# Performance work log

Hardware: AMD Instinct MI355X
Metric: run time of the kernel (lower is better)

## Reference

```python
import jax, jax.numpy as jnp
import numpy as np

N = 10000   # num nodes (== num_features, source uses identity features)
H = 4       # attention heads
F = 128     # out_features per head (concat=False -> mean over heads)
E = 320000  # directed edges
SLOPE = 0.2 # PyG GATConv default negative_slope


def setup_inputs() -> dict:
    key = jax.random.key(0)
    ks = jax.random.split(key, 20)
    inp = {}
    inp['x'] = jax.random.normal(ks[0], (N, N), jnp.float32)
    inp['edge_index'] = jax.random.randint(ks[1], (2, E), 0, N, dtype=jnp.int64)
    dims = [N, F, F, F]
    k = 2
    for i, din in enumerate(dims):
        inp[f'W{i}'] = jax.random.normal(ks[k], (din, H * F), jnp.float32) / np.sqrt(din).astype(np.float32); k += 1
        inp[f'as{i}'] = jax.random.normal(ks[k], (H, F), jnp.float32) / np.sqrt(F).astype(np.float32); k += 1
        inp[f'ad{i}'] = jax.random.normal(ks[k], (H, F), jnp.float32) / np.sqrt(F).astype(np.float32); k += 1
        inp[f'b{i}'] = jnp.zeros((F,), jnp.float32)
    return inp


def _gat_layer(x, src, dst, W, a_src, a_dst, b):
    # x: [N, Din]; W: [Din, H*F]; a_src/a_dst: [H, F]; b: [F]
    h = (x @ W).reshape(-1, H, F)                      # [N, H, F]
    al_s = jnp.sum(h * a_src, axis=-1)                 # [N, H]
    al_d = jnp.sum(h * a_dst, axis=-1)                 # [N, H]
    e = jax.nn.leaky_relu(al_s[src] + al_d[dst], SLOPE)  # [E', H]
    # segment softmax over edges grouped by target node
    m = jax.ops.segment_max(e, dst, num_segments=N)    # [N, H]
    ex = jnp.exp(e - m[dst])
    s = jax.ops.segment_sum(ex, dst, num_segments=N)   # [N, H]
    alpha = ex / s[dst]                                 # [E', H]
    msg = h[src] * alpha[:, :, None]                    # [E', H, F]
    out = jax.ops.segment_sum(msg, dst, num_segments=N) # [N, H, F]
    return out.mean(axis=1) + b                         # concat=False: head mean + bias


def reference(x, edge_index, W0, W1, W2, W3, as0, as1, as2, as3,
              ad0, ad1, ad2, ad3, b0, b1, b2, b3):
    # add self-loops once (PyG GATConv add_self_loops=True, same each layer)
    loop = jnp.arange(N, dtype=edge_index.dtype)
    src = jnp.concatenate([edge_index[0], loop])
    dst = jnp.concatenate([edge_index[1], loop])

    h = jax.nn.relu(_gat_layer(x, src, dst, W0, as0, ad0, b0))
    h = jax.nn.relu(_gat_layer(h, src, dst, W1, as1, ad1, b1))
    h = jax.nn.relu(_gat_layer(h, src, dst, W2, as2, ad2, b2))
    z = jnp.tanh(_gat_layer(h, src, dst, W3, as3, ad3, b3))   # encode
    adj_recon = jax.nn.sigmoid(z @ z.T)                       # decode, [N, N]
    return adj_recon, z
```

## Files before the change

### kernel.cpp

```cpp
#include <hip/hip_runtime.h>

#define N_ 10000
#define H_ 4
#define F_ 128
#define HF_ 512
#define E_ 320000
#define EN_ 330000

typedef unsigned short u16;
typedef __attribute__((ext_vector_type(8))) short bf16x8;
typedef __attribute__((ext_vector_type(4))) float f32x4;

__device__ __forceinline__ u16 f2b1(float f) {
  return (u16)((__float_as_uint(f) + 0x8000u) >> 16);
}
__device__ __forceinline__ unsigned int f2b2(float a, float b) {
  unsigned int ua = __float_as_uint(a) + 0x8000u;
  unsigned int ub = __float_as_uint(b) + 0x8000u;
  return (ua >> 16) | (ub & 0xffff0000u);
}
__device__ __forceinline__ float b2f(u16 u) {
  return __uint_as_float(((unsigned int)u) << 16);
}
__device__ __forceinline__ void async_cp16(const void* g, void* l) {
  __builtin_amdgcn_global_load_lds((__attribute__((address_space(1))) void*)g,
                                   (__attribute__((address_space(3))) void*)l,
                                   16, 0, 0);
}

__global__ void transpose_f2b(const float* __restrict__ in, u16* __restrict__ out,
                              int R, int C) {
  __shared__ float t[32][33];
  int bx = blockIdx.x * 32, by = blockIdx.y * 32;
  int tx = threadIdx.x, ty = threadIdx.y;
#pragma unroll
  for (int i = 0; i < 32; i += 8) {
    int r = by + ty + i, c = bx + tx;
    if (r < R && c < C) t[ty + i][tx] = in[(size_t)r * C + c];
  }
  __syncthreads();
#pragma unroll
  for (int i = 0; i < 32; i += 8) {
    int c = bx + ty + i, r = by + tx;
    if (r < R && c < C) out[(size_t)c * R + r] = f2b1(t[tx][ty + i]);
  }
}

__global__ void zero_k(int* __restrict__ p, int n) {
  int t = blockIdx.x * blockDim.x + threadIdx.x;
  if (t < n) p[t] = 0;
}
__global__ void hist_k(const int* __restrict__ ei, int* __restrict__ cnt) {
  int t = blockIdx.x * blockDim.x + threadIdx.x;
  if (t >= EN_) return;
  int d = (t < E_) ? ei[E_ + t] : (t - E_);
  atomicAdd(&cnt[d], 1);
}
__global__ void scan_k(const int* __restrict__ cnt, int* __restrict__ rp) {
  __shared__ int l[1024];
  const int CH = 10;
  int t = threadIdx.x;
  int base = t * CH;
  int loc[CH];
  int s = 0;
#pragma unroll
  for (int i = 0; i < CH; ++i) {
    int idx = base + i;
    int c = (idx < N_) ? cnt[idx] : 0;
    loc[i] = s; s += c;
  }
  l[t] = s;
  __syncthreads();
  for (int off = 1; off < 1024; off <<= 1) {
    int v = (t >= off) ? l[t - off] : 0;
    __syncthreads();
    l[t] += v;
    __syncthreads();
  }
  int cb = (t == 0) ? 0 : l[t - 1];
#pragma unroll
  for (int i = 0; i < CH; ++i) {
    int idx = base + i;
    if (idx < N_) rp[idx] = cb + loc[i];
  }
  if (t == 1023) rp[N_] = l[1023];
}
__global__ void fill_k(const int* __restrict__ ei, const int* __restrict__ rp,
                       int* __restrict__ fl, int* __restrict__ csrc) {
  int t = blockIdx.x * blockDim.x + threadIdx.x;
  if (t >= EN_) return;
  int s, d;
  if (t < E_) { s = ei[t]; d = ei[E_ + t]; } else { s = d = t - E_; }
  int pos = rp[d] + atomicAdd(&fl[d], 1);
  csrc[pos] = s;
}

#define MFMA_STEP()                                                           \
  {                                                                           \
    bf16x8 af[4], bv[4];                                                      \
    _Pragma("unroll") for (int i = 0; i < 4; ++i)                             \
        af[i] = *(const bf16x8*)&As[(wm + i * 16 + l16) * 32 + quad * 8];     \
    _Pragma("unroll") for (int j = 0; j < 4; ++j)                             \
        bv[j] = *(const bf16x8*)&Bs[(wn + j * 16 + l16) * 32 + quad * 8];     \
    _Pragma("unroll") for (int i = 0; i < 4; ++i)                             \
        _Pragma("unroll") for (int j = 0; j < 4; ++j)                         \
            acc[i][j] = __builtin_amdgcn_mfma_f32_16x16x32_bf16(              \
                af[i], bv[j], acc[i][j], 0, 0, 0);                            \
  }

template <int ASRC, int MODE, int SPLIT>
__global__ __launch_bounds__(256) void gemm_k(const void* __restrict__ Av,
                                              const u16* __restrict__ Bt,
                                              float* __restrict__ C,
                                              int M, int Nc, int K) {
  __shared__ u16 As[128 * 32];
  __shared__ u16 Bs[128 * 32];
  const int tid = threadIdx.x;
  const int lane = tid & 63, wave = tid >> 6;
  const int wm = (wave >> 1) * 64, wn = (wave & 1) * 64;
  const int l16 = lane & 15, quad = lane >> 4;
  const int mBase = blockIdx.y * 128, nBase = blockIdx.x * 128;
  const int r0 = tid >> 2, kk = (tid & 3) * 8;

  int k0 = 0, k1 = K;
  if (SPLIT) {
    int Kper = ((K + (int)gridDim.z - 1) / (int)gridDim.z + 31) & ~31;
    k0 = blockIdx.z * Kper;
    k1 = min(K, k0 + Kper);
    if (k0 > k1) k0 = k1;
  }
  const int len = k1 - k0;

  const u16* Ab = (const u16*)Av;
  const float* Af = (const float*)Av;

  size_t ar0 = (size_t)min(mBase + r0, M - 1);
  size_t ar1 = (size_t)min(mBase + r0 + 64, M - 1);
  size_t br0 = (size_t)min(nBase + r0, Nc - 1);
  size_t br1 = (size_t)min(nBase + r0 + 64, Nc - 1);
  const u16* pb0 = Bt + br0 * (size_t)K + k0 + kk;
  const u16* pb1 = Bt + br1 * (size_t)K + k0 + kk;
  const u16* pa0 = Ab + ar0 * (size_t)K + k0 + kk;
  const u16* pa1 = Ab + ar1 * (size_t)K + k0 + kk;
  const float* pf0 = Af + ar0 * (size_t)K + k0 + kk;
  const float* pf1 = Af + ar1 * (size_t)K + k0 + kk;
  u16* lA0 = As + wave * 512;
  u16* lA1 = As + 2048 + wave * 512;
  u16* lB0 = Bs + wave * 512;
  u16* lB1 = Bs + 2048 + wave * 512;

  f32x4 acc[4][4];
  f32x4 zr = {0.f, 0.f, 0.f, 0.f};
#pragma unroll
  for (int i = 0; i < 4; ++i)
#pragma unroll
    for (int j = 0; j < 4; ++j) acc[i][j] = zr;

  const int Lmain = len & ~31;
  for (int kb = 0; kb < Lmain; kb += 32) {
    async_cp16(pb0 + kb, lB0);
    async_cp16(pb1 + kb, lB1);
    if (ASRC == 0) {
      async_cp16(pa0 + kb, lA0);
      async_cp16(pa1 + kb, lA1);
    } else {
      float4 x0 = *(const float4*)(pf0 + kb);
      float4 x1 = *(const float4*)(pf0 + kb + 4);
      float4 x2 = *(const float4*)(pf1 + kb);
      float4 x3 = *(const float4*)(pf1 + kb + 4);
      uint4 u0 = make_uint4(f2b2(x0.x, x0.y), f2b2(x0.z, x0.w),
                            f2b2(x1.x, x1.y), f2b2(x1.z, x1.w));
      uint4 u1 = make_uint4(f2b2(x2.x, x2.y), f2b2(x2.z, x2.w),
                            f2b2(x3.x, x3.y), f2b2(x3.z, x3.w));
      *(uint4*)&As[r0 * 32 + kk] = u0;
      *(uint4*)&As[(r0 + 64) * 32 + kk] = u1;
    }
    __syncthreads();
    MFMA_STEP();
    __syncthreads();
  }
  if (len & 31) {
#pragma unroll
    for (int c = 0; c < 2; ++c) {
      size_t gr = c ? ar1 : ar0;
      size_t gb = c ? br1 : br0;
      int lrow = r0 + c * 64;
#pragma unroll
      for (int j = 0; j < 8; ++j) {
        int k = k0 + Lmain + kk + j;
        u16 av = 0, bvv = 0;
        if (k < k1) {
          av = (ASRC == 1) ? f2b1(Af[gr * (size_t)K + k]) : Ab[gr * (size_t)K + k];
          bvv = Bt[gb * (size_t)K + k];
        }
        As[lrow * 32 + kk + j] = av;
        Bs[lrow * 32 + kk + j] = bvv;
      }
    }
    __syncthreads();
    MFMA_STEP();
  }

  float* Cw = SPLIT ? (C + (size_t)blockIdx.z * (size_t)M * (size_t)Nc) : C;
#pragma unroll
  for (int i = 0; i < 4; ++i)
#pragma unroll
    for (int j = 0; j < 4; ++j)
#pragma unroll
      for (int r = 0; r < 4; ++r) {
        int row = mBase + wm + i * 16 + quad * 4 + r;
        int col = nBase + wn + j * 16 + l16;
        if (row < M && col < Nc) {
          float v = acc[i][j][r];
          if (!SPLIT && MODE == 1) v = 1.f / (1.f + __expf(-v));
          Cw[(size_t)row * Nc + col] = v;
        }
      }
}

__global__ __launch_bounds__(256) void reduce_k(const float* __restrict__ part,
                                                float* __restrict__ out,
                                                int nq, int S) {
  int t = blockIdx.x * blockDim.x + threadIdx.x;
  if (t >= nq) return;
  size_t stride = (size_t)nq * 4;
  float4 s = ((const float4*)part)[t];
#pragma unroll 1
  for (int z = 1; z < S; ++z) {
    float4 v = *(const float4*)(part + (size_t)z * stride + (size_t)t * 4);
    s.x += v.x; s.y += v.y; s.z += v.z; s.w += v.w;
  }
  ((float4*)out)[t] = s;
}

__global__ __launch_bounds__(256) void prep_k(const float* __restrict__ h,
                                              const float* __restrict__ asv,
                                              const float* __restrict__ adv,
                                              u16* __restrict__ h2,
                                              float* __restrict__ als,
                                              float* __restrict__ ald) {
  int wave = threadIdx.x >> 6, lane = threadIdx.x & 63;
  int node = blockIdx.x * 4 + wave;
  if (node >= N_) return;
  const float* hp = h + (size_t)node * HF_;
  float4 v0 = ((const float4*)hp)[lane * 2];
  float4 v1 = ((const float4*)hp)[lane * 2 + 1];
  float vv[8] = {v0.x, v0.y, v0.z, v0.w, v1.x, v1.y, v1.z, v1.w};
  uint4 pk = make_uint4(f2b2(vv[0], vv[1]), f2b2(vv[2], vv[3]),
                        f2b2(vv[4], vv[5]), f2b2(vv[6], vv[7]));
  *(uint4*)&h2[(size_t)node * HF_ + lane * 8] = pk;
  float4 a0 = ((const float4*)(asv + lane * 8))[0];
  float4 a1 = ((const float4*)(asv + lane * 8))[1];
  float4 d0 = ((const float4*)(adv + lane * 8))[0];
  float4 d1 = ((const float4*)(adv + lane * 8))[1];
  float aa[8] = {a0.x, a0.y, a0.z, a0.w, a1.x, a1.y, a1.z, a1.w};
  float dd[8] = {d0.x, d0.y, d0.z, d0.w, d1.x, d1.y, d1.z, d1.w};
  float ss = 0.f, sd = 0.f;
#pragma unroll
  for (int j = 0; j < 8; ++j) {
    ss += vv[j] * aa[j];
    sd += vv[j] * dd[j];
  }
#pragma unroll
  for (int m = 1; m <= 8; m <<= 1) {
    ss += __shfl_xor(ss, m, 64);
    sd += __shfl_xor(sd, m, 64);
  }
  if ((lane & 15) == 0) {
    int hh = lane >> 4;
    als[node * 4 + hh] = ss;
    ald[node * 4 + hh] = sd;
  }
}

__global__ __launch_bounds__(256) void agg_k(const u16* __restrict__ h2,
                                             const float* __restrict__ als,
                                             const float* __restrict__ ald,
                                             const int* __restrict__ rp,
                                             const int* __restrict__ csrc,
                                             const float* __restrict__ bias,
                                             u16* __restrict__ xout,
                                             float* __restrict__ z32, int act) {
  __shared__ float red[1024];
  __shared__ float sh[512];
  int n = blockIdx.x, t = threadIdx.x;
  int start = rp[n], end = rp[n + 1];
  int hh = t >> 6;
  float4 ad4 = *(const float4*)&ald[n * 4];
  float adh[4] = {ad4.x, ad4.y, ad4.z, ad4.w};
  float lm[4] = {-1e30f, -1e30f, -1e30f, -1e30f};
  for (int j = start + t; j < end; j += 256) {
    int s = csrc[j];
    float4 a4 = *(const float4*)&als[s * 4];
    float e0 = a4.x + adh[0]; e0 = e0 > 0.f ? e0 : 0.2f * e0;
    float e1 = a4.y + adh[1]; e1 = e1 > 0.f ? e1 : 0.2f * e1;
    float e2 = a4.z + adh[2]; e2 = e2 > 0.f ? e2 : 0.2f * e2;
    float e3 = a4.w + adh[3]; e3 = e3 > 0.f ? e3 : 0.2f * e3;
    lm[0] = fmaxf(lm[0], e0); lm[1] = fmaxf(lm[1], e1);
    lm[2] = fmaxf(lm[2], e2); lm[3] = fmaxf(lm[3], e3);
  }
#pragma unroll
  for (int h = 0; h < 4; ++h) red[t * 4 + h] = lm[h];
  __syncthreads();
  for (int off = 128; off >= 1; off >>= 1) {
    if (t < off) {
#pragma unroll
      for (int h = 0; h < 4; ++h)
        red[t * 4 + h] = fmaxf(red[t * 4 + h], red[(t + off) * 4 + h]);
    }
    __syncthreads();
  }
  float mh = red[hh];
  float adhh = adh[hh];
  float acc0 = 0.f, acc1 = 0.f, ssum = 0.f;
  for (int j = start; j < end; ++j) {
    int s = csrc[j];
    float e = als[s * 4 + hh] + adhh;
    e = e > 0.f ? e : 0.2f * e;
    float w = __expf(e - mh);
    ssum += w;
    unsigned int p = *(const unsigned int*)&h2[(size_t)s * HF_ + 2 * t];
    acc0 += w * b2f((u16)(p & 0xffffu));
    acc1 += w * b2f((u16)(p >> 16));
  }
  float inv = 1.f / ssum;
  sh[2 * t] = acc0 * inv;
  sh[2 * t + 1] = acc1 * inv;
  __syncthreads();
  if (t < 64) {
    int f0 = 2 * t, f1 = 2 * t + 1;
    float w0 = 0.25f * (sh[f0] + sh[128 + f0] + sh[256 + f0] + sh[384 + f0]) + bias[f0];
    float w1 = 0.25f * (sh[f1] + sh[128 + f1] + sh[256 + f1] + sh[384 + f1]) + bias[f1];
    if (act) { w0 = tanhf(w0); w1 = tanhf(w1); }
    else     { w0 = fmaxf(w0, 0.f); w1 = fmaxf(w1, 0.f); }
    if (z32) {
      z32[(size_t)n * F_ + f0] = w0;
      z32[(size_t)n * F_ + f1] = w1;
    }
    *(unsigned int*)&xout[(size_t)n * F_ + f0] = f2b2(w0, w1);
  }
}

extern "C" void kernel_launch(void* const* d_in, const int* in_sizes, int n_in,
                              void* d_out, int out_size, void* d_ws, size_t ws_size,
                              hipStream_t stream) {
  const float* x = (const float*)d_in[0];
  const int* ei = (const int*)d_in[1];
  const float* W[4]; const float* asv[4]; const float* adv[4]; const float* bv[4];
  for (int i = 0; i < 4; ++i) {
    W[i]   = (const float*)d_in[2 + i * 4];
    asv[i] = (const float*)d_in[3 + i * 4];
    adv[i] = (const float*)d_in[4 + i * 4];
    bv[i]  = (const float*)d_in[5 + i * 4];
  }
  float* out_adj = (float*)d_out;
  float* out_z = out_adj + (size_t)N_ * N_;

  char* w = (char*)d_ws;
  size_t o = 0;
  auto carve = [&](size_t bytes) {
    char* p = w + o;
    o += (bytes + 255) & ~(size_t)255;
    return p;
  };
  float* hbuf = (float*)carve((size_t)N_ * HF_ * 4);
  u16* h2   = (u16*)carve((size_t)N_ * HF_ * 2);
  u16* wt0  = (u16*)carve((size_t)HF_ * N_ * 2);
  u16* wt1  = (u16*)carve((size_t)HF_ * F_ * 2);
  u16* wt2  = (u16*)carve((size_t)HF_ * F_ * 2);
  u16* wt3  = (u16*)carve((size_t)HF_ * F_ * 2);
  float* als = (float*)carve((size_t)N_ * 4 * 4);
  float* ald = (float*)carve((size_t)N_ * 4 * 4);
  u16* bufA = (u16*)carve((size_t)N_ * F_ * 2);
  u16* bufB = (u16*)carve((size_t)N_ * F_ * 2);
  u16* zb   = (u16*)carve((size_t)N_ * F_ * 2);
  int* cnt = (int*)carve((size_t)2 * N_ * 4);
  int* fl = cnt + N_;
  int* rowptr = (int*)carve((size_t)(N_ + 1) * 4);
  int* csrc = (int*)carve((size_t)EN_ * 4);

  const int SPLITK = 8;
  float* part = out_adj;

  dim3 tb(32, 8);
  transpose_f2b<<<dim3(16, 313), tb, 0, stream>>>(W[0], wt0, N_, HF_);
  transpose_f2b<<<dim3(16, 4), tb, 0, stream>>>(W[1], wt1, F_, HF_);
  transpose_f2b<<<dim3(16, 4), tb, 0, stream>>>(W[2], wt2, F_, HF_);
  transpose_f2b<<<dim3(16, 4), tb, 0, stream>>>(W[3], wt3, F_, HF_);

  zero_k<<<(2 * N_ + 255) / 256, 256, 0, stream>>>(cnt, 2 * N_);
  hist_k<<<(EN_ + 255) / 256, 256, 0, stream>>>(ei, cnt);
  scan_k<<<1, 1024, 0, stream>>>(cnt, rowptr);
  fill_k<<<(EN_ + 255) / 256, 256, 0, stream>>>(ei, rowptr, fl, csrc);

  const u16* wt[4] = {wt0, wt1, wt2, wt3};
  const u16* xin[4] = {nullptr, bufA, bufB, bufA};
  u16* xout[4] = {bufA, bufB, bufA, zb};

  for (int l = 0; l < 4; ++l) {
    if (l == 0) {
      gemm_k<1, 0, 1><<<dim3(4, 79, SPLITK), 256, 0, stream>>>(x, wt0, part,
                                                               N_, HF_, N_);
      int nq = N_ * HF_ / 4;
      reduce_k<<<(nq + 255) / 256, 256, 0, stream>>>(part, hbuf, nq, SPLITK);
    } else {
      gemm_k<0, 0, 0><<<dim3(4, 79), 256, 0, stream>>>(xin[l], wt[l], hbuf,
                                                       N_, HF_, F_);
    }
    prep_k<<<N_ / 4, 256, 0, stream>>>(hbuf, asv[l], adv[l], h2, als, ald);
    agg_k<<<N_, 256, 0, stream>>>(h2, als, ald, rowptr, csrc, bv[l], xout[l],
                                  (l == 3) ? out_z : nullptr, (l == 3) ? 1 : 0);
  }

  gemm_k<0, 1, 0><<<dim3(79, 79), 256, 0, stream>>>(zb, zb, out_adj, N_, N_, F_);
}
```

Before: 1.421 ms.

## Pre-convert input to bf16 and fuse split-K reduction into prep kernel

Adds a standalone kernel that converts the large fp32 input matrix to bf16 once, so the first-layer GEMM loads A tiles with async global-to-LDS copies instead of converting fp32 inline per tile. The split-K partial sums are now reduced inside the prep kernel, which removes the separate reduce kernel and its extra full-size write and read. Scratch buffers are placed in the output adjacency buffer, which the final GEMM overwrites. The cost is an extra full pass over the input for conversion.

```diff
diff --git a/kernel.cpp b/kernel.cpp
--- a/kernel.cpp
+++ b/kernel.cpp
@@ -26,6 +26,19 @@
   __builtin_amdgcn_global_load_lds((__attribute__((address_space(1))) void*)g,
                                    (__attribute__((address_space(3))) void*)l,
                                    16, 0, 0);
+}
+
+__global__ __launch_bounds__(256) void convert_k(const float* __restrict__ in,
+                                                 u16* __restrict__ out, long nq) {
+  long t = (long)blockIdx.x * blockDim.x + threadIdx.x;
+  long stride = (long)gridDim.x * blockDim.x;
+  for (long i = t; i < nq; i += stride) {
+    float4 a = ((const float4*)in)[i * 2];
+    float4 b = ((const float4*)in)[i * 2 + 1];
+    uint4 p = make_uint4(f2b2(a.x, a.y), f2b2(a.z, a.w),
+                         f2b2(b.x, b.y), f2b2(b.z, b.w));
+    ((uint4*)out)[i] = p;
+  }
 }
 
 __global__ void transpose_f2b(const float* __restrict__ in, u16* __restrict__ out,
@@ -108,8 +121,8 @@
                 af[i], bv[j], acc[i][j], 0, 0, 0);                            \
   }
 
-template <int ASRC, int MODE, int SPLIT>
-__global__ __launch_bounds__(256) void gemm_k(const void* __restrict__ Av,
+template <int MODE, int SPLIT>
+__global__ __launch_bounds__(256) void gemm_k(const u16* __restrict__ Ab,
                                               const u16* __restrict__ Bt,
                                               float* __restrict__ C,
                                               int M, int Nc, int K) {
@@ -131,9 +144,6 @@
   }
   const int len = k1 - k0;
 
-  const u16* Ab = (const u16*)Av;
-  const float* Af = (const float*)Av;
-
   size_t ar0 = (size_t)min(mBase + r0, M - 1);
   size_t ar1 = (size_t)min(mBase + r0 + 64, M - 1);
   size_t br0 = (size_t)min(nBase + r0, Nc - 1);
@@ -142,8 +152,6 @@
   const u16* pb1 = Bt + br1 * (size_t)K + k0 + kk;
   const u16* pa0 = Ab + ar0 * (size_t)K + k0 + kk;
   const u16* pa1 = Ab + ar1 * (size_t)K + k0 + kk;
-  const float* pf0 = Af + ar0 * (size_t)K + k0 + kk;
-  const float* pf1 = Af + ar1 * (size_t)K + k0 + kk;
   u16* lA0 = As + wave * 512;
   u16* lA1 = As + 2048 + wave * 512;
   u16* lB0 = Bs + wave * 512;
@@ -160,21 +168,8 @@
   for (int kb = 0; kb < Lmain; kb += 32) {
     async_cp16(pb0 + kb, lB0);
     async_cp16(pb1 + kb, lB1);
-    if (ASRC == 0) {
-      async_cp16(pa0 + kb, lA0);
-      async_cp16(pa1 + kb, lA1);
-    } else {
-      float4 x0 = *(const float4*)(pf0 + kb);
-      float4 x1 = *(const float4*)(pf0 + kb + 4);
-      float4 x2 = *(const float4*)(pf1 + kb);
-      float4 x3 = *(const float4*)(pf1 + kb + 4);
-      uint4 u0 = make_uint4(f2b2(x0.x, x0.y), f2b2(x0.z, x0.w),
-                            f2b2(x1.x, x1.y), f2b2(x1.z, x1.w));
-      uint4 u1 = make_uint4(f2b2(x2.x, x2.y), f2b2(x2.z, x2.w),
-                            f2b2(x3.x, x3.y), f2b2(x3.z, x3.w));
-      *(uint4*)&As[r0 * 32 + kk] = u0;
-      *(uint4*)&As[(r0 + 64) * 32 + kk] = u1;
-    }
+    async_cp16(pa0 + kb, lA0);
+    async_cp16(pa1 + kb, lA1);
     __syncthreads();
     MFMA_STEP();
     __syncthreads();
@@ -190,7 +185,7 @@
         int k = k0 + Lmain + kk + j;
         u16 av = 0, bvv = 0;
         if (k < k1) {
-          av = (ASRC == 1) ? f2b1(Af[gr * (size_t)K + k]) : Ab[gr * (size_t)K + k];
+          av = Ab[gr * (size_t)K + k];
           bvv = Bt[gb * (size_t)K + k];
         }
         As[lrow * 32 + kk + j] = av;
@@ -218,33 +213,27 @@
       }
 }
 
-__global__ __launch_bounds__(256) void reduce_k(const float* __restrict__ part,
-                                                float* __restrict__ out,
-                                                int nq, int S) {
-  int t = blockIdx.x * blockDim.x + threadIdx.x;
-  if (t >= nq) return;
-  size_t stride = (size_t)nq * 4;
-  float4 s = ((const float4*)part)[t];
-#pragma unroll 1
-  for (int z = 1; z < S; ++z) {
-    float4 v = *(const float4*)(part + (size_t)z * stride + (size_t)t * 4);
-    s.x += v.x; s.y += v.y; s.z += v.z; s.w += v.w;
-  }
-  ((float4*)out)[t] = s;
-}
-
 __global__ __launch_bounds__(256) void prep_k(const float* __restrict__ h,
                                               const float* __restrict__ asv,
                                               const float* __restrict__ adv,
                                               u16* __restrict__ h2,
                                               float* __restrict__ als,
-                                              float* __restrict__ ald) {
+                                              float* __restrict__ ald,
+                                              int S, size_t zstride) {
   int wave = threadIdx.x >> 6, lane = threadIdx.x & 63;
   int node = blockIdx.x * 4 + wave;
   if (node >= N_) return;
   const float* hp = h + (size_t)node * HF_;
   float4 v0 = ((const float4*)hp)[lane * 2];
   float4 v1 = ((const float4*)hp)[lane * 2 + 1];
+#pragma unroll 1
+  for (int z = 1; z < S; ++z) {
+    const float* pp = hp + (size_t)z * zstride;
+    float4 w0 = ((const float4*)pp)[lane * 2];
+    float4 w1 = ((const float4*)pp)[lane * 2 + 1];
+    v0.x += w0.x; v0.y += w0.y; v0.z += w0.z; v0.w += w0.w;
+    v1.x += w1.x; v1.y += w1.y; v1.z += w1.z; v1.w += w1.w;
+  }
   float vv[8] = {v0.x, v0.y, v0.z, v0.w, v1.x, v1.y, v1.z, v1.w};
   uint4 pk = make_uint4(f2b2(vv[0], vv[1]), f2b2(vv[2], vv[3]),
                         f2b2(vv[4], vv[5]), f2b2(vv[6], vv[7]));
@@ -380,7 +369,8 @@
   int* csrc = (int*)carve((size_t)EN_ * 4);
 
   const int SPLITK = 8;
-  float* part = out_adj;
+  u16* xb = (u16*)out_adj;
+  float* part = out_adj + (size_t)N_ * N_ / 2;
 
   dim3 tb(32, 8);
   transpose_f2b<<<dim3(16, 313), tb, 0, stream>>>(W[0], wt0, N_, HF_);
@@ -388,6 +378,8 @@
   transpose_f2b<<<dim3(16, 4), tb, 0, stream>>>(W[2], wt2, F_, HF_);
   transpose_f2b<<<dim3(16, 4), tb, 0, stream>>>(W[3], wt3, F_, HF_);
 
+  convert_k<<<2048, 256, 0, stream>>>(x, xb, (long)N_ * N_ / 8);
+
   zero_k<<<(2 * N_ + 255) / 256, 256, 0, stream>>>(cnt, 2 * N_);
   hist_k<<<(EN_ + 255) / 256, 256, 0, stream>>>(ei, cnt);
   scan_k<<<1, 1024, 0, stream>>>(cnt, rowptr);
@@ -399,18 +391,19 @@
 
   for (int l = 0; l < 4; ++l) {
     if (l == 0) {
-      gemm_k<1, 0, 1><<<dim3(4, 79, SPLITK), 256, 0, stream>>>(x, wt0, part,
-                                                               N_, HF_, N_);
-      int nq = N_ * HF_ / 4;
-      reduce_k<<<(nq + 255) / 256, 256, 0, stream>>>(part, hbuf, nq, SPLITK);
+      gemm_k<0, 1><<<dim3(4, 79, SPLITK), 256, 0, stream>>>(xb, wt0, part,
+                                                            N_, HF_, N_);
+      prep_k<<<N_ / 4, 256, 0, stream>>>(part, asv[0], adv[0], h2, als, ald,
+                                         SPLITK, (size_t)N_ * HF_);
     } else {
-      gemm_k<0, 0, 0><<<dim3(4, 79), 256, 0, stream>>>(xin[l], wt[l], hbuf,
-                                                       N_, HF_, F_);
+      gemm_k<0, 0><<<dim3(4, 79), 256, 0, stream>>>(xin[l], wt[l], hbuf,
+                                                    N_, HF_, F_);
+      prep_k<<<N_ / 4, 256, 0, stream>>>(hbuf, asv[l], adv[l], h2, als, ald,
+                                         1, 0);
     }
-    prep_k<<<N_ / 4, 256, 0, stream>>>(hbuf, asv[l], adv[l], h2, als, ald);
     agg_k<<<N_, 256, 0, stream>>>(h2, als, ald, rowptr, csrc, bv[l], xout[l],
                                   (l == 3) ? out_z : nullptr, (l == 3) ? 1 : 0);
   }
 
-  gemm_k<0, 1, 0><<<dim3(79, 79), 256, 0, stream>>>(zb, zb, out_adj, N_, N_, F_);
-}
+  gemm_k<1, 0><<<dim3(79, 79), 256, 0, stream>>>(zb, zb, out_adj, N_, N_, F_);
+}
```

New measurement: 1.508 ms. 1.06x slower.

## Double-buffer GEMM shared tiles and fold split-K reduction into prep kernel

Applied to the files above, without the earlier changes.

The GEMM kernel now uses two shared-memory tile buffers, so the next K-tile is loaded (async copies, or fp32 loads converted to bf16 after the MFMAs) while the current tile is computed. This leaves one barrier per iteration instead of two. The separate split-K reduce kernel is removed: prep_k sums the partial slices directly, saving a full write and reread of the N×512 fp32 intermediate and one launch. Shared memory per block doubles, which may lower occupancy.

```diff
diff --git a/kernel.cpp b/kernel.cpp
--- a/kernel.cpp
+++ b/kernel.cpp
@@ -95,13 +95,13 @@
   csrc[pos] = s;
 }
 
-#define MFMA_STEP()                                                           \
+#define MFMA_TILE(ASP, BSP)                                                   \
   {                                                                           \
     bf16x8 af[4], bv[4];                                                      \
     _Pragma("unroll") for (int i = 0; i < 4; ++i)                             \
-        af[i] = *(const bf16x8*)&As[(wm + i * 16 + l16) * 32 + quad * 8];     \
+        af[i] = *(const bf16x8*)&(ASP)[(wm + i * 16 + l16) * 32 + quad * 8];  \
     _Pragma("unroll") for (int j = 0; j < 4; ++j)                             \
-        bv[j] = *(const bf16x8*)&Bs[(wn + j * 16 + l16) * 32 + quad * 8];     \
+        bv[j] = *(const bf16x8*)&(BSP)[(wn + j * 16 + l16) * 32 + quad * 8];  \
     _Pragma("unroll") for (int i = 0; i < 4; ++i)                             \
         _Pragma("unroll") for (int j = 0; j < 4; ++j)                         \
             acc[i][j] = __builtin_amdgcn_mfma_f32_16x16x32_bf16(              \
@@ -113,8 +113,8 @@
                                               const u16* __restrict__ Bt,
                                               float* __restrict__ C,
                                               int M, int Nc, int K) {
-  __shared__ u16 As[128 * 32];
-  __shared__ u16 Bs[128 * 32];
+  __shared__ u16 As[2][128 * 32];
+  __shared__ u16 Bs[2][128 * 32];
   const int tid = threadIdx.x;
   const int lane = tid & 63, wave = tid >> 6;
   const int wm = (wave >> 1) * 64, wn = (wave & 1) * 64;
@@ -144,10 +144,8 @@
   const u16* pa1 = Ab + ar1 * (size_t)K + k0 + kk;
   const float* pf0 = Af + ar0 * (size_t)K + k0 + kk;
   const float* pf1 = Af + ar1 * (size_t)K + k0 + kk;
-  u16* lA0 = As + wave * 512;
-  u16* lA1 = As + 2048 + wave * 512;
-  u16* lB0 = Bs + wave * 512;
-  u16* lB1 = Bs + 2048 + wave * 512;
+  const int lofsA = wave * 512;
+  const int lofsA2 = 2048 + wave * 512;
 
   f32x4 acc[4][4];
   f32x4 zr = {0.f, 0.f, 0.f, 0.f};
@@ -157,28 +155,59 @@
     for (int j = 0; j < 4; ++j) acc[i][j] = zr;
 
   const int Lmain = len & ~31;
-  for (int kb = 0; kb < Lmain; kb += 32) {
-    async_cp16(pb0 + kb, lB0);
-    async_cp16(pb1 + kb, lB1);
+  const int nt = Lmain >> 5;
+
+  if (nt > 0) {
+    async_cp16(pb0, Bs[0] + lofsA);
+    async_cp16(pb1, Bs[0] + lofsA2);
     if (ASRC == 0) {
-      async_cp16(pa0 + kb, lA0);
-      async_cp16(pa1 + kb, lA1);
+      async_cp16(pa0, As[0] + lofsA);
+      async_cp16(pa1, As[0] + lofsA2);
     } else {
-      float4 x0 = *(const float4*)(pf0 + kb);
-      float4 x1 = *(const float4*)(pf0 + kb + 4);
-      float4 x2 = *(const float4*)(pf1 + kb);
-      float4 x3 = *(const float4*)(pf1 + kb + 4);
-      uint4 u0 = make_uint4(f2b2(x0.x, x0.y), f2b2(x0.z, x0.w),
-                            f2b2(x1.x, x1.y), f2b2(x1.z, x1.w));
-      uint4 u1 = make_uint4(f2b2(x2.x, x2.y), f2b2(x2.z, x2.w),
-                            f2b2(x3.x, x3.y), f2b2(x3.z, x3.w));
-      *(uint4*)&As[r0 * 32 + kk] = u0;
-      *(uint4*)&As[(r0 + 64) * 32 + kk] = u1;
-    }
-    __syncthreads();
-    MFMA_STEP();
-    __syncthreads();
-  }
+      float4 x0 = *(const float4*)(pf0);
+      float4 x1 = *(const float4*)(pf0 + 4);
+      float4 x2 = *(const float4*)(pf1);
+      float4 x3 = *(const float4*)(pf1 + 4);
+      *(uint4*)&As[0][r0 * 32 + kk] =
+          make_uint4(f2b2(x0.x, x0.y), f2b2(x0.z, x0.w),
+                     f2b2(x1.x, x1.y), f2b2(x1.z, x1.w));
+      *(uint4*)&As[0][(r0 + 64) * 32 + kk] =
+          make_uint4(f2b2(x2.x, x2.y), f2b2(x2.z, x2.w),
+                     f2b2(x3.x, x3.y), f2b2(x3.z, x3.w));
+    }
+    __syncthreads();
+  }
+
+  for (int t = 0; t < nt; ++t) {
+    const int cur = t & 1, nxt = cur ^ 1;
+    const int kb = (t + 1) << 5;
+    const bool pre = (t + 1 < nt);
+    float4 x0, x1, x2, x3;
+    if (pre) {
+      async_cp16(pb0 + kb, Bs[nxt] + lofsA);
+      async_cp16(pb1 + kb, Bs[nxt] + lofsA2);
+      if (ASRC == 0) {
+        async_cp16(pa0 + kb, As[nxt] + lofsA);
+        async_cp16(pa1 + kb, As[nxt] + lofsA2);
+      } else {
+        x0 = *(const float4*)(pf0 + kb);
+        x1 = *(const float4*)(pf0 + kb + 4);
+        x2 = *(const float4*)(pf1 + kb);
+        x3 = *(const float4*)(pf1 + kb + 4);
+      }
+    }
+    MFMA_TILE(As[cur], Bs[cur]);
+    if (ASRC == 1 && pre) {
+      *(uint4*)&As[nxt][r0 * 32 + kk] =
+          make_uint4(f2b2(x0.x, x0.y), f2b2(x0.z, x0.w),
+                     f2b2(x1.x, x1.y), f2b2(x1.z, x1.w));
+      *(uint4*)&As[nxt][(r0 + 64) * 32 + kk] =
+          make_uint4(f2b2(x2.x, x2.y), f2b2(x2.z, x2.w),
+                     f2b2(x3.x, x3.y), f2b2(x3.z, x3.w));
+    }
+    __syncthreads();
+  }
+
   if (len & 31) {
 #pragma unroll
     for (int c = 0; c < 2; ++c) {
@@ -193,12 +222,12 @@
           av = (ASRC == 1) ? f2b1(Af[gr * (size_t)K + k]) : Ab[gr * (size_t)K + k];
           bvv = Bt[gb * (size_t)K + k];
         }
-        As[lrow * 32 + kk + j] = av;
-        Bs[lrow * 32 + kk + j] = bvv;
+        As[0][lrow * 32 + kk + j] = av;
+        Bs[0][lrow * 32 + kk + j] = bvv;
       }
     }
     __syncthreads();
-    MFMA_STEP();
+    MFMA_TILE(As[0], Bs[0]);
   }
 
   float* Cw = SPLIT ? (C + (size_t)blockIdx.z * (size_t)M * (size_t)Nc) : C;
@@ -218,33 +247,27 @@
       }
 }
 
-__global__ __launch_bounds__(256) void reduce_k(const float* __restrict__ part,
-                                                float* __restrict__ out,
-                                                int nq, int S) {
-  int t = blockIdx.x * blockDim.x + threadIdx.x;
-  if (t >= nq) return;
-  size_t stride = (size_t)nq * 4;
-  float4 s = ((const float4*)part)[t];
-#pragma unroll 1
-  for (int z = 1; z < S; ++z) {
-    float4 v = *(const float4*)(part + (size_t)z * stride + (size_t)t * 4);
-    s.x += v.x; s.y += v.y; s.z += v.z; s.w += v.w;
-  }
-  ((float4*)out)[t] = s;
-}
-
 __global__ __launch_bounds__(256) void prep_k(const float* __restrict__ h,
                                               const float* __restrict__ asv,
                                               const float* __restrict__ adv,
                                               u16* __restrict__ h2,
                                               float* __restrict__ als,
-                                              float* __restrict__ ald) {
+                                              float* __restrict__ ald,
+                                              int S, size_t zstride) {
   int wave = threadIdx.x >> 6, lane = threadIdx.x & 63;
   int node = blockIdx.x * 4 + wave;
   if (node >= N_) return;
   const float* hp = h + (size_t)node * HF_;
   float4 v0 = ((const float4*)hp)[lane * 2];
   float4 v1 = ((const float4*)hp)[lane * 2 + 1];
+#pragma unroll 1
+  for (int z = 1; z < S; ++z) {
+    const float* pp = hp + (size_t)z * zstride;
+    float4 w0 = ((const float4*)pp)[lane * 2];
+    float4 w1 = ((const float4*)pp)[lane * 2 + 1];
+    v0.x += w0.x; v0.y += w0.y; v0.z += w0.z; v0.w += w0.w;
+    v1.x += w1.x; v1.y += w1.y; v1.z += w1.z; v1.w += w1.w;
+  }
   float vv[8] = {v0.x, v0.y, v0.z, v0.w, v1.x, v1.y, v1.z, v1.w};
   uint4 pk = make_uint4(f2b2(vv[0], vv[1]), f2b2(vv[2], vv[3]),
                         f2b2(vv[4], vv[5]), f2b2(vv[6], vv[7]));
@@ -401,13 +424,14 @@
     if (l == 0) {
       gemm_k<1, 0, 1><<<dim3(4, 79, SPLITK), 256, 0, stream>>>(x, wt0, part,
                                                                N_, HF_, N_);
-      int nq = N_ * HF_ / 4;
-      reduce_k<<<(nq + 255) / 256, 256, 0, stream>>>(part, hbuf, nq, SPLITK);
+      prep_k<<<N_ / 4, 256, 0, stream>>>(part, asv[0], adv[0], h2, als, ald,
+                                         SPLITK, (size_t)N_ * HF_);
     } else {
       gemm_k<0, 0, 0><<<dim3(4, 79), 256, 0, stream>>>(xin[l], wt[l], hbuf,
                                                        N_, HF_, F_);
-    }
-    prep_k<<<N_ / 4, 256, 0, stream>>>(hbuf, asv[l], adv[l], h2, als, ald);
+      prep_k<<<N_ / 4, 256, 0, stream>>>(hbuf, asv[l], adv[l], h2, als, ald,
+                                         1, 0);
+    }
     agg_k<<<N_, 256, 0, stream>>>(h2, als, ald, rowptr, csrc, bv[l], xout[l],
                                   (l == 3) ? out_z : nullptr, (l == 3) ? 1 : 0);
   }
```

New measurement: 1.470 ms. +3.5%, slower.

## Fuse split-K reduction into prep kernel and remap split-K block order

Applied to the files above, without the earlier changes.

Removes the separate split-K reduce kernel by having prep_k sum the partial GEMM slices while converting to bf16 and computing attention logits. This avoids writing and rereading the full fp32 layer-0 projection. The split-K GEMM also remaps its flat block index so that the k-slice index varies fastest, which changes the L2 access pattern across concurrently running blocks. The remap may reduce reuse of A tiles across column blocks.

```diff
diff --git a/kernel.cpp b/kernel.cpp
--- a/kernel.cpp
+++ b/kernel.cpp
@@ -119,13 +119,22 @@
   const int lane = tid & 63, wave = tid >> 6;
   const int wm = (wave >> 1) * 64, wn = (wave & 1) * 64;
   const int l16 = lane & 15, quad = lane >> 4;
-  const int mBase = blockIdx.y * 128, nBase = blockIdx.x * 128;
   const int r0 = tid >> 2, kk = (tid & 3) * 8;
+
+  int xb = blockIdx.x, yb = blockIdx.y, zb = 0;
+  if (SPLIT) {
+    int flat = blockIdx.x + gridDim.x * (blockIdx.y + gridDim.y * blockIdx.z);
+    zb = flat % (int)gridDim.z;
+    int r = flat / (int)gridDim.z;
+    xb = r % (int)gridDim.x;
+    yb = r / (int)gridDim.x;
+  }
+  const int mBase = yb * 128, nBase = xb * 128;
 
   int k0 = 0, k1 = K;
   if (SPLIT) {
     int Kper = ((K + (int)gridDim.z - 1) / (int)gridDim.z + 31) & ~31;
-    k0 = blockIdx.z * Kper;
+    k0 = zb * Kper;
     k1 = min(K, k0 + Kper);
     if (k0 > k1) k0 = k1;
   }
@@ -201,7 +210,7 @@
     MFMA_STEP();
   }
 
-  float* Cw = SPLIT ? (C + (size_t)blockIdx.z * (size_t)M * (size_t)Nc) : C;
+  float* Cw = SPLIT ? (C + (size_t)zb * (size_t)M * (size_t)Nc) : C;
 #pragma unroll
   for (int i = 0; i < 4; ++i)
 #pragma unroll
@@ -218,33 +227,27 @@
       }
 }
 
-__global__ __launch_bounds__(256) void reduce_k(const float* __restrict__ part,
-                                                float* __restrict__ out,
-                                                int nq, int S) {
-  int t = blockIdx.x * blockDim.x + threadIdx.x;
-  if (t >= nq) return;
-  size_t stride = (size_t)nq * 4;
-  float4 s = ((const float4*)part)[t];
-#pragma unroll 1
-  for (int z = 1; z < S; ++z) {
-    float4 v = *(const float4*)(part + (size_t)z * stride + (size_t)t * 4);
-    s.x += v.x; s.y += v.y; s.z += v.z; s.w += v.w;
-  }
-  ((float4*)out)[t] = s;
-}
-
 __global__ __launch_bounds__(256) void prep_k(const float* __restrict__ h,
                                               const float* __restrict__ asv,
                                               const float* __restrict__ adv,
                                               u16* __restrict__ h2,
                                               float* __restrict__ als,
-                                              float* __restrict__ ald) {
+                                              float* __restrict__ ald,
+                                              int S, size_t zstride) {
   int wave = threadIdx.x >> 6, lane = threadIdx.x & 63;
   int node = blockIdx.x * 4 + wave;
   if (node >= N_) return;
   const float* hp = h + (size_t)node * HF_;
   float4 v0 = ((const float4*)hp)[lane * 2];
   float4 v1 = ((const float4*)hp)[lane * 2 + 1];
+#pragma unroll 1
+  for (int z = 1; z < S; ++z) {
+    const float* pp = hp + (size_t)z * zstride;
+    float4 w0 = ((const float4*)pp)[lane * 2];
+    float4 w1 = ((const float4*)pp)[lane * 2 + 1];
+    v0.x += w0.x; v0.y += w0.y; v0.z += w0.z; v0.w += w0.w;
+    v1.x += w1.x; v1.y += w1.y; v1.z += w1.z; v1.w += w1.w;
+  }
   float vv[8] = {v0.x, v0.y, v0.z, v0.w, v1.x, v1.y, v1.z, v1.w};
   uint4 pk = make_uint4(f2b2(vv[0], vv[1]), f2b2(vv[2], vv[3]),
                         f2b2(vv[4], vv[5]), f2b2(vv[6], vv[7]));
@@ -401,13 +404,14 @@
     if (l == 0) {
       gemm_k<1, 0, 1><<<dim3(4, 79, SPLITK), 256, 0, stream>>>(x, wt0, part,
                                                                N_, HF_, N_);
-      int nq = N_ * HF_ / 4;
-      reduce_k<<<(nq + 255) / 256, 256, 0, stream>>>(part, hbuf, nq, SPLITK);
+      prep_k<<<N_ / 4, 256, 0, stream>>>(part, asv[0], adv[0], h2, als, ald,
+                                         SPLITK, (size_t)N_ * HF_);
     } else {
       gemm_k<0, 0, 0><<<dim3(4, 79), 256, 0, stream>>>(xin[l], wt[l], hbuf,
                                                        N_, HF_, F_);
+      prep_k<<<N_ / 4, 256, 0, stream>>>(hbuf, asv[l], adv[l], h2, als, ald,
+                                         1, 0);
     }
-    prep_k<<<N_ / 4, 256, 0, stream>>>(hbuf, asv[l], adv[l], h2, als, ald);
     agg_k<<<N_, 256, 0, stream>>>(h2, als, ald, rowptr, csrc, bv[l], xout[l],
                                   (l == 3) ? out_z : nullptr, (l == 3) ? 1 : 0);
   }
```

New measurement: 1.382 ms. -2.7%, faster.
